# Optimization experiments

Measured on AMD Instinct MI355X. Metric: run time of the kernel, lower is better.

## Reference

```python
import jax, jax.numpy as jnp
import numpy as np

N_LIG, N_REC = 4096, 16384
E_LIG, E_REC = 65536, 262144
H, OUT, ORIG = 256, 256, 64
EF_LIG, EF_REC = 16, 16
N_SIG = 15
SLOPE = 0.01      # leakyrelu_neg_slope
SKIP_H = 0.5      # skip_weight_h
X_INIT = 0.25     # x_connection_init
SIGMAS = np.asarray(1.5 ** np.arange(N_SIG), dtype=np.float32)  # all_sigmas_dist


def _lrelu(x):
    return jax.nn.leaky_relu(x, SLOPE)


def _mlp2(x, w1, b1, w2, b2):
    # Linear -> LeakyReLU -> (Identity norm) -> Linear
    return _lrelu(x @ w1 + b1) @ w2 + b2


def _seg_mean(vals, idx, n):
    s = jax.ops.segment_sum(vals, idx, num_segments=n)
    d = jax.ops.segment_sum(jnp.ones((vals.shape[0], 1), vals.dtype), idx, num_segments=n)
    return s / jnp.maximum(d, 1.0)


def _rbf(x_rel):
    # multi-sigma RBF of squared edge distance: exp(-|x_rel|^2 / sigma), 15 sigmas
    d2 = jnp.sum(x_rel * x_rel, axis=1, keepdims=True)        # [E,1]
    return jnp.exp(-d2 / jnp.asarray(SIGMAS, x_rel.dtype))    # [E,15]


def _cross_attention(q, k, v, mask):
    a = mask * (q @ k.T) - 1000.0 * (1.0 - mask)
    return jax.nn.softmax(a, axis=1) @ v


def setup_inputs():
    key = jax.random.key(0)
    ks = iter(jax.random.split(key, 64))

    def rn(*shape):
        return jax.random.normal(next(ks), shape, dtype=jnp.float32)

    def w(fi, fo):
        return rn(fi, fo) / np.float32(np.sqrt(fi))

    e_in_l = 2 * H + EF_LIG + N_SIG
    e_in_r = 2 * H + EF_REC + N_SIG
    n_in = ORIG + H + OUT
    z = lambda d: jnp.zeros((d,), jnp.float32)
    inp = dict(
        coords_lig=rn(N_LIG, 3), h_feats_lig=rn(N_LIG, H),
        orig_lig_feats=rn(N_LIG, ORIG), orig_coords_lig=rn(N_LIG, 3),
        coords_rec=rn(N_REC, 3), h_feats_rec=rn(N_REC, H),
        orig_rec_feats=rn(N_REC, ORIG), orig_coords_rec=rn(N_REC, 3),
        mask=jnp.ones((N_LIG, N_REC), jnp.float32),
        lig_edge_feat=rn(E_LIG, EF_LIG), rec_edge_feat=rn(E_REC, EF_REC),
        lig_src=jax.random.randint(next(ks), (E_LIG,), 0, N_LIG),
        lig_dst=jax.random.randint(next(ks), (E_LIG,), 0, N_LIG),
        rec_src=jax.random.randint(next(ks), (E_REC,), 0, N_REC),
        rec_dst=jax.random.randint(next(ks), (E_REC,), 0, N_REC),
        lig_edge_w1=w(e_in_l, OUT), lig_edge_b1=z(OUT), lig_edge_w2=w(OUT, OUT), lig_edge_b2=z(OUT),
        rec_edge_w1=w(e_in_r, OUT), rec_edge_b1=z(OUT), rec_edge_w2=w(OUT, OUT), rec_edge_b2=z(OUT),
        att_q_lig_w=w(H, H), att_k_lig_w=w(H, H), att_v_lig_w=w(H, H),
        att_q_rec_w=w(H, H), att_k_rec_w=w(H, H), att_v_rec_w=w(H, H),
        node_lig_w1=w(n_in, H), node_lig_b1=z(H), node_lig_w2=w(H, OUT), node_lig_b2=z(OUT),
        node_rec_w1=w(n_in, H), node_rec_b1=z(H), node_rec_w2=w(H, OUT), node_rec_b2=z(OUT),
        coords_lig_w1=w(OUT, OUT), coords_lig_b1=z(OUT), coords_lig_w2=w(OUT, 1), coords_lig_b2=z(1),
        coords_rec_w1=w(OUT, OUT), coords_rec_b1=z(OUT), coords_rec_w2=w(OUT, 1), coords_rec_b2=z(1),
    )
    return inp


def reference(coords_lig, h_feats_lig, orig_lig_feats, orig_coords_lig,
              coords_rec, h_feats_rec, orig_rec_feats, orig_coords_rec,
              mask, lig_edge_feat, rec_edge_feat,
              lig_src, lig_dst, rec_src, rec_dst,
              lig_edge_w1, lig_edge_b1, lig_edge_w2, lig_edge_b2,
              rec_edge_w1, rec_edge_b1, rec_edge_w2, rec_edge_b2,
              att_q_lig_w, att_k_lig_w, att_v_lig_w,
              att_q_rec_w, att_k_rec_w, att_v_rec_w,
              node_lig_w1, node_lig_b1, node_lig_w2, node_lig_b2,
              node_rec_w1, node_rec_b1, node_rec_w2, node_rec_b2,
              coords_lig_w1, coords_lig_b1, coords_lig_w2, coords_lig_b2,
              coords_rec_w1, coords_rec_b1, coords_rec_w2, coords_rec_b2):
    n_lig, n_rec = coords_lig.shape[0], coords_rec.shape[0]
    # edge messages: gather endpoint features + edge attrs + RBF(dist)
    x_rel_l = coords_lig[lig_src] - coords_lig[lig_dst]                       # [E_lig,3]
    msg_l = _mlp2(jnp.concatenate([h_feats_lig[lig_src], h_feats_lig[lig_dst],
                                   lig_edge_feat, _rbf(x_rel_l)], axis=1),
                  lig_edge_w1, lig_edge_b1, lig_edge_w2, lig_edge_b2)         # [E_lig,OUT]
    x_rel_r = coords_rec[rec_src] - coords_rec[rec_dst]
    msg_r = _mlp2(jnp.concatenate([h_feats_rec[rec_src], h_feats_rec[rec_dst],
                                   rec_edge_feat, _rbf(x_rel_r)], axis=1),
                  rec_edge_w1, rec_edge_b1, rec_edge_w2, rec_edge_b2)         # [E_rec,OUT]
    # cross attention between ligand and receptor node sets
    cross_l = _cross_attention(_lrelu(h_feats_lig @ att_q_lig_w),
                               _lrelu(h_feats_rec @ att_k_rec_w),
                               h_feats_rec @ att_v_rec_w, mask)               # [N_lig,H]
    cross_r = _cross_attention(_lrelu(h_feats_rec @ att_q_rec_w),
                               _lrelu(h_feats_lig @ att_k_lig_w),
                               h_feats_lig @ att_v_lig_w, mask.T)             # [N_rec,H]
    # equivariant coordinate updates: mean over incoming edges of x_rel * coords_mlp(msg)
    x_upd_l = _seg_mean(x_rel_l * _mlp2(msg_l, coords_lig_w1, coords_lig_b1,
                                        coords_lig_w2, coords_lig_b2), lig_dst, n_lig)
    x_upd_r = _seg_mean(x_rel_r * _mlp2(msg_r, coords_rec_w1, coords_rec_b1,
                                        coords_rec_w2, coords_rec_b2), rec_dst, n_rec)
    x_ev_l = X_INIT * orig_coords_lig + (1.0 - X_INIT) * coords_lig + x_upd_l
    x_ev_r = X_INIT * orig_coords_rec + (1.0 - X_INIT) * coords_rec + x_upd_r
    # node feature updates: cat(aggr_msg, cross_att, original features) -> MLP + skip
    aggr_l = _seg_mean(msg_l, lig_dst, n_lig)
    aggr_r = _seg_mean(msg_r, rec_dst, n_rec)
    h_l = SKIP_H * _mlp2(jnp.concatenate([aggr_l, cross_l, orig_lig_feats], axis=1),
                         node_lig_w1, node_lig_b1, node_lig_w2, node_lig_b2) \
          + (1.0 - SKIP_H) * h_feats_lig
    h_r = SKIP_H * _mlp2(jnp.concatenate([aggr_r, cross_r, orig_rec_feats], axis=1),
                         node_rec_w1, node_rec_b1, node_rec_w2, node_rec_b2) \
          + (1.0 - SKIP_H) * h_feats_rec
    return (x_ev_l, h_l, x_ev_r, h_r)
```

## Files before the change

kernel.cpp:

```cpp
#include <hip/hip_runtime.h>
#include <hip/hip_bf16.h>


#define N_LIG   4096
#define N_REC   16384
#define E_LIG_N 65536
#define E_REC_N 262144
#define HD      256
#define ORIGD   64
#define EFD     16
#define NSIG    15
#define EIN     543
#define XP      552
#define XPN     584
#define XPP     264
#define FP      264

typedef __bf16 bf16x8 __attribute__((ext_vector_type(8)));
typedef float  f32x4  __attribute__((ext_vector_type(4)));

__device__ __forceinline__ float lrelu(float x) { return x > 0.f ? x : 0.01f * x; }
__device__ __forceinline__ unsigned short f2bu(float f) {
    __hip_bfloat16 h = __float2bfloat16(f);
    return *reinterpret_cast<unsigned short*>(&h);
}

__device__ __forceinline__ void glds16(const void* g, void* l) {
    __builtin_amdgcn_global_load_lds(
        (const __attribute__((address_space(1))) void*)g,
        (__attribute__((address_space(3))) void*)l,
        16, 0, 0);
}

__device__ __forceinline__ void stage_tile(
    const __hip_bfloat16* g, unsigned short* l, int wave, int lane)
{
    #pragma unroll
    for (int i = 0; i < 2; ++i) {
        const __hip_bfloat16* gp = g + (size_t)(i * 512 + wave * 64 + lane) * 8;
        unsigned short* lp = l + (i * 512 + wave * 64) * 8;
        glds16(gp, lp);
    }
}

__device__ __forceinline__ void mfma_gemm(
    const unsigned short* sA, int pitch,
    const __hip_bfloat16* Wswz, int KS, int lane, f32x4 acc[2][4])
{
    const int col = lane & 15, quad = lane >> 4;
    const unsigned short* a0p = sA + (size_t)col * pitch + quad * 8;
    const unsigned short* a1p = sA + (size_t)(16 + col) * pitch + quad * 8;
    const __hip_bfloat16* wp = Wswz + lane * 8;

    bf16x8 bE[4], bO[4], aE0, aE1, aO0, aO1;
    #pragma unroll
    for (int nt = 0; nt < 4; ++nt) {
        bE[nt] = *reinterpret_cast<const bf16x8*>(wp + (size_t)nt * KS * 512);
        bO[nt] = *reinterpret_cast<const bf16x8*>(wp + ((size_t)nt * KS + 1) * 512);
    }
    aE0 = *reinterpret_cast<const bf16x8*>(a0p);
    aE1 = *reinterpret_cast<const bf16x8*>(a1p);
    aO0 = *reinterpret_cast<const bf16x8*>(a0p + 32);
    aO1 = *reinterpret_cast<const bf16x8*>(a1p + 32);

    int ks = 0;
    for (; ks + 2 <= KS; ks += 2) {
        #pragma unroll
        for (int nt = 0; nt < 4; ++nt) {
            acc[0][nt] = __builtin_amdgcn_mfma_f32_16x16x32_bf16(aE0, bE[nt], acc[0][nt], 0, 0, 0);
            acc[1][nt] = __builtin_amdgcn_mfma_f32_16x16x32_bf16(aE1, bE[nt], acc[1][nt], 0, 0, 0);
        }
        if (ks + 2 < KS) {
            #pragma unroll
            for (int nt = 0; nt < 4; ++nt)
                bE[nt] = *reinterpret_cast<const bf16x8*>(
                    wp + ((size_t)nt * KS + ks + 2) * 512);
            aE0 = *reinterpret_cast<const bf16x8*>(a0p + (ks + 2) * 32);
            aE1 = *reinterpret_cast<const bf16x8*>(a1p + (ks + 2) * 32);
        }
        #pragma unroll
        for (int nt = 0; nt < 4; ++nt) {
            acc[0][nt] = __builtin_amdgcn_mfma_f32_16x16x32_bf16(aO0, bO[nt], acc[0][nt], 0, 0, 0);
            acc[1][nt] = __builtin_amdgcn_mfma_f32_16x16x32_bf16(aO1, bO[nt], acc[1][nt], 0, 0, 0);
        }
        if (ks + 3 < KS) {
            #pragma unroll
            for (int nt = 0; nt < 4; ++nt)
                bO[nt] = *reinterpret_cast<const bf16x8*>(
                    wp + ((size_t)nt * KS + ks + 3) * 512);
            aO0 = *reinterpret_cast<const bf16x8*>(a0p + (ks + 3) * 32);
            aO1 = *reinterpret_cast<const bf16x8*>(a1p + (ks + 3) * 32);
        }
    }
    if (ks < KS) {
        #pragma unroll
        for (int nt = 0; nt < 4; ++nt) {
            acc[0][nt] = __builtin_amdgcn_mfma_f32_16x16x32_bf16(aE0, bE[nt], acc[0][nt], 0, 0, 0);
            acc[1][nt] = __builtin_amdgcn_mfma_f32_16x16x32_bf16(aE1, bE[nt], acc[1][nt], 0, 0, 0);
        }
    }
}

__global__ void zero_kernel(float* __restrict__ p, int n) {
    int i = blockIdx.x * 256 + threadIdx.x;
    if (i < n) p[i] = 0.f;
}

__global__ void f2b_kernel(const float* __restrict__ src,
                           __hip_bfloat16* __restrict__ dst, int n8) {
    const int i = blockIdx.x * 256 + threadIdx.x;
    if (i >= n8) return;
    const float4 a = *reinterpret_cast<const float4*>(src + (size_t)i * 8);
    const float4 b = *reinterpret_cast<const float4*>(src + (size_t)i * 8 + 4);
    ushort4 u0 = { f2bu(a.x), f2bu(a.y), f2bu(a.z), f2bu(a.w) };
    ushort4 u1 = { f2bu(b.x), f2bu(b.y), f2bu(b.z), f2bu(b.w) };
    unsigned short* d = (unsigned short*)dst + (size_t)i * 8;
    *reinterpret_cast<ushort4*>(d)     = u0;
    *reinterpret_cast<ushort4*>(d + 4) = u1;
}

__global__ void hist_kernel(const int* __restrict__ dst, int* __restrict__ hist, int n) {
    int i = blockIdx.x * 256 + threadIdx.x;
    if (i < n) atomicAdd(&hist[dst[i]], 1);
}

__global__ __launch_bounds__(256) void scan_kernel(
    const int* __restrict__ hist, int* __restrict__ cur,
    float* __restrict__ cntf, int n)
{
    __shared__ int part[256];
    const int tid = threadIdx.x;
    const int per = n >> 8;
    const int base = tid * per;
    int s = 0;
    for (int i = 0; i < per; ++i) s += hist[base + i];
    part[tid] = s;
    __syncthreads();
    #pragma unroll
    for (int off = 1; off < 256; off <<= 1) {
        int v = (tid >= off) ? part[tid - off] : 0;
        __syncthreads();
        part[tid] += v;
        __syncthreads();
    }
    int run = part[tid] - s;
    for (int i = 0; i < per; ++i) {
        const int h = hist[base + i];
        cur[base + i]  = run;
        cntf[base + i] = (float)h;
        run += h;
    }
}

__global__ void scatter_kernel(const int* __restrict__ dst, int* __restrict__ cur,
                               int* __restrict__ elist, int n) {
    int i = blockIdx.x * 256 + threadIdx.x;
    if (i < n) { int p = atomicAdd(&cur[dst[i]], 1); elist[p] = i; }
}

__global__ void wt_swz(const float* __restrict__ src,
                       __hip_bfloat16* __restrict__ dst, int K, int KS) {
    const int g  = blockIdx.x / KS;
    const int ks = blockIdx.x % KS;
    for (int i = threadIdx.x; i < 512; i += 256) {
        const int lane = i >> 3, j = i & 7;
        const int n = g * 16 + (lane & 15);
        const int k = ks * 32 + (lane >> 4) * 8 + j;
        const float v = (k < K) ? src[(size_t)k * 256 + n] : 0.f;
        dst[((size_t)(g * KS + ks) * 64 + lane) * 8 + j] = __float2bfloat16(v);
    }
}

__global__ __launch_bounds__(256, 4) void edge_mfma(
    const float* __restrict__ coords, const __hip_bfloat16* __restrict__ hb,
    const __hip_bfloat16* __restrict__ efb,
    const int* __restrict__ src, const int* __restrict__ dst,
    const int* __restrict__ elist,
    const __hip_bfloat16* __restrict__ W1s, const float* __restrict__ b1,
    const __hip_bfloat16* __restrict__ W2s, const float* __restrict__ b2,
    const __hip_bfloat16* __restrict__ Wc1s, const float* __restrict__ bc1,
    const float* __restrict__ wc2v, const float* __restrict__ bc2,
    float* __restrict__ aggr, float* __restrict__ xsum)
{
    __shared__ unsigned short sX[32][XP];
    __shared__ float sXrel[32][3];
    __shared__ int   sDst[32];
    __shared__ int   sSrc[32];
    __shared__ int   sE[32];
    __shared__ float sRedW[4][32];
    __shared__ float sPv[32];

    const int tid  = threadIdx.x;
    const int lane = tid & 63;
    const int wave = tid >> 6;
    const int col  = lane & 15;
    const int quad = lane >> 4;
    const int e0   = blockIdx.x * 32;

    if (tid < 32) {
        const int e = elist[e0 + tid];
        const int s = src[e], d = dst[e];
        sE[tid] = e; sSrc[tid] = s; sDst[tid] = d;
        float d2 = 0.f;
        #pragma unroll
        for (int c = 0; c < 3; ++c) {
            const float xr = coords[s * 3 + c] - coords[d * 3 + c];
            sXrel[tid][c] = xr;
            d2 += xr * xr;
        }
        float sig = 1.0f;
        #pragma unroll
        for (int si = 0; si < NSIG; ++si) {
            sX[tid][528 + si] = f2bu(__expf(-d2 / sig));
            sig *= 1.5f;
        }
        sX[tid][543] = 0;
    }
    __syncthreads();

    for (int i = tid; i < 32 * 64; i += 256) {
        const int row = i >> 6, c = i & 63;
        const int node = (c < 32) ? sSrc[row] : sDst[row];
        const int chunk = c & 31;
        *reinterpret_cast<uint4*>(&sX[row][(c < 32 ? 0 : 256) + chunk * 8]) =
            *reinterpret_cast<const uint4*>(&hb[(size_t)node * HD + chunk * 8]);
    }
    if (tid < 64) {
        const int row = tid >> 1, hh = tid & 1;
        *reinterpret_cast<uint4*>(&sX[row][512 + hh * 8]) =
            *reinterpret_cast<const uint4*>(&efb[(size_t)sE[row] * EFD + hh * 8]);
    }
    __syncthreads();

    f32x4 acc[2][4];
    f32x4 macc[2][4];

    #pragma unroll
    for (int nt = 0; nt < 4; ++nt) {
        const float bv = b1[wave * 64 + nt * 16 + col];
        acc[0][nt] = { bv, bv, bv, bv };
        acc[1][nt] = { bv, bv, bv, bv };
    }
    mfma_gemm(&sX[0][0], XP, W1s + (size_t)(wave * 4) * 17 * 512, 17, lane, acc);
    __syncthreads();
    #pragma unroll
    for (int mt = 0; mt < 2; ++mt)
        #pragma unroll
        for (int nt = 0; nt < 4; ++nt)
            #pragma unroll
            for (int r = 0; r < 4; ++r)
                sX[mt * 16 + quad * 4 + r][wave * 64 + nt * 16 + col] =
                    f2bu(lrelu(acc[mt][nt][r]));
    __syncthreads();

    #pragma unroll
    for (int nt = 0; nt < 4; ++nt) {
        const float bv = b2[wave * 64 + nt * 16 + col];
        macc[0][nt] = { bv, bv, bv, bv };
        macc[1][nt] = { bv, bv, bv, bv };
    }
    mfma_gemm(&sX[0][0], XP, W2s + (size_t)(wave * 4) * 8 * 512, 8, lane, macc);
    __syncthreads();
    #pragma unroll
    for (int mt = 0; mt < 2; ++mt)
        #pragma unroll
        for (int nt = 0; nt < 4; ++nt)
            #pragma unroll
            for (int r = 0; r < 4; ++r)
                sX[mt * 16 + quad * 4 + r][wave * 64 + nt * 16 + col] =
                    f2bu(macc[mt][nt][r]);
    __syncthreads();

    #pragma unroll
    for (int nt = 0; nt < 4; ++nt) {
        const float bv = bc1[wave * 64 + nt * 16 + col];
        acc[0][nt] = { bv, bv, bv, bv };
        acc[1][nt] = { bv, bv, bv, bv };
    }
    mfma_gemm(&sX[0][0], XP, Wc1s + (size_t)(wave * 4) * 8 * 512, 8, lane, acc);
    float w2l[4];
    #pragma unroll
    for (int nt = 0; nt < 4; ++nt) w2l[nt] = wc2v[wave * 64 + nt * 16 + col];
    #pragma unroll
    for (int mt = 0; mt < 2; ++mt) {
        float pr[4] = { 0.f, 0.f, 0.f, 0.f };
        #pragma unroll
        for (int nt = 0; nt < 4; ++nt)
            #pragma unroll
            for (int r = 0; r < 4; ++r)
                pr[r] += lrelu(acc[mt][nt][r]) * w2l[nt];
        #pragma unroll
        for (int r = 0; r < 4; ++r) {
            #pragma unroll
            for (int off = 1; off < 16; off <<= 1) pr[r] += __shfl_xor(pr[r], off);
        }
        if (col == 0)
            #pragma unroll
            for (int r = 0; r < 4; ++r)
                sRedW[wave][mt * 16 + quad * 4 + r] = pr[r];
    }
    __syncthreads();

    float* sF = reinterpret_cast<float*>(&sX[0][0]);
    #pragma unroll
    for (int mt = 0; mt < 2; ++mt)
        #pragma unroll
        for (int nt = 0; nt < 4; ++nt)
            #pragma unroll
            for (int r = 0; r < 4; ++r)
                sF[(mt * 16 + quad * 4 + r) * FP + wave * 64 + nt * 16 + col] =
                    macc[mt][nt][r];
    if (tid < 32)
        sPv[tid] = sRedW[0][tid] + sRedW[1][tid] + sRedW[2][tid] + sRedW[3][tid]
                 + bc2[0];
    __syncthreads();

    {
        const int c = tid;
        float av = 0.f;
        int dprev = sDst[0];
        for (int row = 0; row < 32; ++row) {
            const int d = sDst[row];
            if (d != dprev) {
                atomicAdd(&aggr[(size_t)dprev * HD + c], av);
                av = 0.f; dprev = d;
            }
// ... 79 lines not shown
            for (int r = 0; r < 4; ++r)
                sXn[mt * 16 + quad * 4 + r][wave * 64 + nt * 16 + col] =
                    f2bu(lrelu(acc[mt][nt][r]));
    __syncthreads();

    #pragma unroll
    for (int nt = 0; nt < 4; ++nt) {
        const float bv = b2[wave * 64 + nt * 16 + col];
        acc[0][nt] = { bv, bv, bv, bv };
        acc[1][nt] = { bv, bv, bv, bv };
    }
    mfma_gemm(&sXn[0][0], XPN, WN2s + (size_t)(wave * 4) * 8 * 512, 8, lane, acc);
    #pragma unroll
    for (int mt = 0; mt < 2; ++mt)
        #pragma unroll
        for (int nt = 0; nt < 4; ++nt)
            #pragma unroll
            for (int r = 0; r < 4; ++r) {
                const int g = r0 + mt * 16 + quad * 4 + r;
                const int n = wave * 64 + nt * 16 + col;
                out[(size_t)g * HD + n] =
                    0.5f * acc[mt][nt][r] + 0.5f * hfeat[(size_t)g * HD + n];
            }
}

__global__ __launch_bounds__(256, 4) void qkv_proj(
    const __hip_bfloat16* __restrict__ Xb,
    const __hip_bfloat16* __restrict__ Wq, const __hip_bfloat16* __restrict__ Wk,
    const __hip_bfloat16* __restrict__ Wv,
    __hip_bfloat16* __restrict__ Q, __hip_bfloat16* __restrict__ Kz,
    __hip_bfloat16* __restrict__ Vz)
{
    __shared__ unsigned short sXp[32][XPP];
    const int tid  = threadIdx.x;
    const int lane = tid & 63;
    const int wave = tid >> 6;
    const int col  = lane & 15;
    const int quad = lane >> 4;
    const int r0   = blockIdx.x * 32;

    for (int i = tid; i < 32 * 32; i += 256) {
        const int row = i >> 5, c = i & 31;
        *reinterpret_cast<uint4*>(&sXp[row][c * 8]) =
            *reinterpret_cast<const uint4*>(&Xb[(size_t)(r0 + row) * HD + c * 8]);
    }
    __syncthreads();

    f32x4 acc[2][4];
    #pragma unroll
    for (int p = 0; p < 3; ++p) {
        const __hip_bfloat16* Ws = (p == 0) ? Wq : (p == 1) ? Wk : Wv;
        #pragma unroll
        for (int nt = 0; nt < 4; ++nt) {
            acc[0][nt] = { 0.f, 0.f, 0.f, 0.f };
            acc[1][nt] = { 0.f, 0.f, 0.f, 0.f };
        }
        mfma_gemm(&sXp[0][0], XPP, Ws + (size_t)(wave * 4) * 8 * 512, 8, lane, acc);
        #pragma unroll
        for (int mt = 0; mt < 2; ++mt)
            #pragma unroll
            for (int nt = 0; nt < 4; ++nt)
                #pragma unroll
                for (int r = 0; r < 4; ++r) {
                    float v = acc[mt][nt][r];
                    const int row = r0 + mt * 16 + quad * 4 + r;
                    const int c   = wave * 64 + nt * 16 + col;
                    if (p == 0) {
                        Q[(size_t)row * HD + c] = __float2bfloat16(lrelu(v));
                    } else if (p == 1) {
                        const int kt = row >> 4, rr = row & 15;
                        const int s  = c >> 5, cc8 = (c >> 3) & 3, j = c & 7;
                        Kz[(size_t)(kt * 8 + s) * 512 + (cc8 * 16 + rr) * 8 + j] =
                            __float2bfloat16(lrelu(v));
                    } else {
                        const int jt = row >> 5, rowin = row & 31;
                        const int dt = c >> 4, cc = c & 15;
                        Vz[((size_t)(jt * 16 + dt) * 64 + (rowin >> 3) * 16 + cc) * 8
                           + (rowin & 7)] = __float2bfloat16(v);
                    }
                }
    }
}

__device__ __forceinline__ void load_mask(
    const float* __restrict__ maskG, int transposed, int R0, int j0,
    int wave, int quad, int col, float mv[2][4])
{
    if (!transposed) {
        #pragma unroll
        for (int t = 0; t < 2; ++t)
            #pragma unroll
            for (int r = 0; r < 4; ++r)
                mv[t][r] = maskG[(size_t)(R0 + wave * 16 + quad * 4 + r) * N_REC
                                 + j0 + col + 16 * t];
    } else {
        #pragma unroll
        for (int t = 0; t < 2; ++t)
            #pragma unroll
            for (int r = 0; r < 4; ++r)
                mv[t][r] = maskG[(size_t)(j0 + col + 16 * t) * N_REC
                                 + R0 + wave * 16 + quad * 4 + r];
    }
}

__device__ __forceinline__ void attn_tile(
    const unsigned short* sK, const unsigned short* sV,
    unsigned short (*sPw)[40], const bf16x8 qf[8], const float mv[2][4],
    int lane, int col, int quad, f32x4 o[16], float m[4], float l[4])
{
    f32x4 sacc[2];
    sacc[0][0]=0.f; sacc[0][1]=0.f; sacc[0][2]=0.f; sacc[0][3]=0.f;
    sacc[1][0]=0.f; sacc[1][1]=0.f; sacc[1][2]=0.f; sacc[1][3]=0.f;
    #pragma unroll
    for (int t = 0; t < 2; ++t) {
        #pragma unroll
        for (int s = 0; s < 8; ++s) {
            bf16x8 kf = *reinterpret_cast<const bf16x8*>(
                &sK[(t * 8 + s) * 512 + lane * 8]);
            sacc[t] = __builtin_amdgcn_mfma_f32_16x16x32_bf16(qf[s], kf, sacc[t], 0, 0, 0);
        }
    }

    float a[2][4];
    #pragma unroll
    for (int t = 0; t < 2; ++t)
        #pragma unroll
        for (int r = 0; r < 4; ++r)
            a[t][r] = mv[t][r] * sacc[t][r] - 1000.f * (1.f - mv[t][r]);

    float lm[4];
    #pragma unroll
    for (int r = 0; r < 4; ++r) lm[r] = fmaxf(a[0][r], a[1][r]);
    float w = lm[0] - m[0];
    #pragma unroll
    for (int r = 1; r < 4; ++r) w = fmaxf(w, lm[r] - m[r]);
    if (!__all(w <= 8.f)) {
        #pragma unroll
        for (int r = 0; r < 4; ++r) {
            float mx = lm[r];
            #pragma unroll
            for (int off = 1; off < 16; off <<= 1)
                mx = fmaxf(mx, __shfl_xor(mx, off));
            const float mn = fmaxf(m[r], mx);
            const float c  = __expf(m[r] - mn);
            m[r] = mn;
            l[r] *= c;
            #pragma unroll
            for (int dt = 0; dt < 16; ++dt) o[dt][r] *= c;
        }
    }

    #pragma unroll
    for (int r = 0; r < 4; ++r) {
        const float p0 = __expf(a[0][r] - m[r]);
        const float p1 = __expf(a[1][r] - m[r]);
        sPw[quad * 4 + r][col]      = f2bu(p0);
        sPw[quad * 4 + r][col + 16] = f2bu(p1);
        l[r] += p0 + p1;
    }

    bf16x8 pf = *reinterpret_cast<const bf16x8*>(&sPw[col][quad * 8]);
    #pragma unroll
    for (int dt = 0; dt < 16; ++dt) {
        bf16x8 vf = *reinterpret_cast<const bf16x8*>(&sV[dt * 512 + lane * 8]);
        o[dt] = __builtin_amdgcn_mfma_f32_16x16x32_bf16(pf, vf, o[dt], 0, 0, 0);
    }
}

__global__ __launch_bounds__(512) void attn_mfma(
    const __hip_bfloat16* __restrict__ Qb, const __hip_bfloat16* __restrict__ Kz,
    const __hip_bfloat16* __restrict__ Vz, const float* __restrict__ maskG,
    float* __restrict__ PO, float* __restrict__ PM, float* __restrict__ PL,
    int M, int chunkKeys, int transposed)
{
    __shared__ unsigned short sKb[2][8192];
    __shared__ unsigned short sVb[2][8192];
    __shared__ unsigned short sP[8][16][40];

    const int tid  = threadIdx.x;
    const int lane = tid & 63;
    const int wave = tid >> 6;
    const int col  = lane & 15;
    const int quad = lane >> 4;
    const int R0   = blockIdx.x * 128;
    const int split = blockIdx.y;
    const int jbase = split * chunkKeys;

    bf16x8 qf[8];
    {
        const __hip_bfloat16* qp =
            Qb + (size_t)(R0 + wave * 16 + col) * HD + quad * 8;
        #pragma unroll
        for (int s = 0; s < 8; ++s)
            qf[s] = *reinterpret_cast<const bf16x8*>(qp + 32 * s);
    }

    f32x4 o[16];
    #pragma unroll
    for (int dt = 0; dt < 16; ++dt) { o[dt][0]=0.f; o[dt][1]=0.f; o[dt][2]=0.f; o[dt][3]=0.f; }
    float m[4], l[4];
    #pragma unroll
    for (int r = 0; r < 4; ++r) { m[r] = -INFINITY; l[r] = 0.f; }

    float mvA[2][4], mvB[2][4];

    stage_tile(Kz + (size_t)jbase * 256, &sKb[0][0], wave, lane);
    stage_tile(Vz + (size_t)jbase * 256, &sVb[0][0], wave, lane);
    load_mask(maskG, transposed, R0, jbase, wave, quad, col, mvA);

    for (int jt = 0; jt < chunkKeys; jt += 64) {
        asm volatile("s_waitcnt vmcnt(0)" ::: "memory");
        __builtin_amdgcn_s_barrier();
        __builtin_amdgcn_sched_barrier(0);
        stage_tile(Kz + (size_t)(jbase + jt + 32) * 256, &sKb[1][0], wave, lane);
        stage_tile(Vz + (size_t)(jbase + jt + 32) * 256, &sVb[1][0], wave, lane);
        load_mask(maskG, transposed, R0, jbase + jt + 32, wave, quad, col, mvB);
        __builtin_amdgcn_sched_barrier(0);
        attn_tile(&sKb[0][0], &sVb[0][0], sP[wave], qf, mvA,
                  lane, col, quad, o, m, l);

        asm volatile("s_waitcnt vmcnt(0)" ::: "memory");
        __builtin_amdgcn_s_barrier();
        __builtin_amdgcn_sched_barrier(0);
        if (jt + 64 < chunkKeys) {
            stage_tile(Kz + (size_t)(jbase + jt + 64) * 256, &sKb[0][0], wave, lane);
            stage_tile(Vz + (size_t)(jbase + jt + 64) * 256, &sVb[0][0], wave, lane);
            load_mask(maskG, transposed, R0, jbase + jt + 64, wave, quad, col, mvA);
        }
        __builtin_amdgcn_sched_barrier(0);
        attn_tile(&sKb[1][0], &sVb[1][0], sP[wave], qf, mvB,
                  lane, col, quad, o, m, l);
    }

    #pragma unroll
    for (int r = 0; r < 4; ++r) {
        #pragma unroll
        for (int off = 1; off < 16; off <<= 1)
            l[r] += __shfl_xor(l[r], off);
    }

    #pragma unroll
    for (int dt = 0; dt < 16; ++dt)
        #pragma unroll
        for (int r = 0; r < 4; ++r) {
            const int row = R0 + wave * 16 + quad * 4 + r;
            PO[((size_t)split * M + row) * HD + dt * 16 + col] = o[dt][r];
        }
    if (col == 0) {
        #pragma unroll
        for (int r = 0; r < 4; ++r) {
            const int row = R0 + wave * 16 + quad * 4 + r;
            PM[(size_t)split * M + row] = m[r];
            PL[(size_t)split * M + row] = l[r];
        }
    }
}

__global__ void attn_combine(
    const float* __restrict__ PO, const float* __restrict__ PM,
    const float* __restrict__ PL, __hip_bfloat16* __restrict__ Out,
    int M, int nchunks)
{
    const int idx = blockIdx.x * 256 + threadIdx.x;
    const int row = idx >> 8;
    float mmax = -INFINITY;
    for (int c = 0; c < nchunks; ++c) mmax = fmaxf(mmax, PM[(size_t)c * M + row]);
    float denom = 0.f, acc = 0.f;
    for (int c = 0; c < nchunks; ++c) {
        const float w = __expf(PM[(size_t)c * M + row] - mmax);
        denom += PL[(size_t)c * M + row] * w;
        acc   += PO[(size_t)c * M * HD + idx] * w;
    }
    Out[idx] = __float2bfloat16(acc / denom);
}

__global__ void coords_fin(
    const float* __restrict__ coords, const float* __restrict__ origc,
    const float* __restrict__ xsum, const float* __restrict__ cnt,
    float* __restrict__ out, int n)
{
    const int i = blockIdx.x * 256 + threadIdx.x;
    if (i >= n * 3) return;
    const int node = i / 3;
    const float inv = 1.f / fmaxf(cnt[node], 1.f);
    out[i] = 0.25f * origc[i] + 0.75f * coords[i] + xsum[i] * inv;
}

extern "C" void kernel_launch(void* const* d_in, const int* in_sizes, int n_in,
                              void* d_out, int out_size, void* d_ws, size_t ws_size,
                              hipStream_t stream)
{
    const float* coords_lig = (const float*)d_in[0];
    const float* h_lig      = (const float*)d_in[1];
    const float* orig_lig   = (const float*)d_in[2];
    const float* origc_lig  = (const float*)d_in[3];
    const float* coords_rec = (const float*)d_in[4];
    const float* h_rec      = (const float*)d_in[5];
    const float* orig_rec   = (const float*)d_in[6];
    const float* origc_rec  = (const float*)d_in[7];
    const float* mask       = (const float*)d_in[8];
    const float* lig_ef     = (const float*)d_in[9];
    const float* rec_ef     = (const float*)d_in[10];
    const int* lig_src = (const int*)d_in[11];
    const int* lig_dst = (const int*)d_in[12];
    const int* rec_src = (const int*)d_in[13];
    const int* rec_dst = (const int*)d_in[14];
    const float* le_w1 = (const float*)d_in[15];
    const float* le_b1 = (const float*)d_in[16];
    const float* le_w2 = (const float*)d_in[17];
    const float* le_b2 = (const float*)d_in[18];
    const float* re_w1 = (const float*)d_in[19];
    const float* re_b1 = (const float*)d_in[20];
    const float* re_w2 = (const float*)d_in[21];
    const float* re_b2 = (const float*)d_in[22];
    const float* aql_w = (const float*)d_in[23];
    const float* akl_w = (const float*)d_in[24];
    const float* avl_w = (const float*)d_in[25];
    const float* aqr_w = (const float*)d_in[26];
    const float* akr_w = (const float*)d_in[27];
    const float* avr_w = (const float*)d_in[28];
    const float* nl_w1 = (const float*)d_in[29];
    const float* nl_b1 = (const float*)d_in[30];
    const float* nl_w2 = (const float*)d_in[31];
    const float* nl_b2 = (const float*)d_in[32];
    const float* nr_w1 = (const float*)d_in[33];
    const float* nr_b1 = (const float*)d_in[34];
    const float* nr_w2 = (const float*)d_in[35];
    const float* nr_b2 = (const float*)d_in[36];
    const float* cl_w1 = (const float*)d_in[37];
    const float* cl_b1 = (const float*)d_in[38];
    const float* cl_w2 = (const float*)d_in[39];
    const float* cl_b2 = (const float*)d_in[40];
    const float* cr_w1 = (const float*)d_in[41];
    const float* cr_b1 = (const float*)d_in[42];
    const float* cr_w2 = (const float*)d_in[43];
    const float* cr_b2 = (const float*)d_in[44];

    float* out = (float*)d_out;
    float* wsf = (float*)d_ws;

    const size_t AGGRL = 0;
    const size_t AGGRR = AGGRL + (size_t)N_LIG * HD;
    const size_t CNTL  = AGGRR + (size_t)N_REC * HD;
    const size_t CNTR  = CNTL + N_LIG;
    const size_t XSUML = CNTR + N_REC;
    const size_t XSUMR = XSUML + (size_t)N_LIG * 3;
    const size_t HISTL = XSUMR + (size_t)N_REC * 3;
    const size_t CURL  = HISTL + N_LIG;
    const size_t HISTR = CURL + N_LIG;
    const size_t CURR  = HISTR + N_REC;
    const size_t ZEND  = CURR + N_REC;
    const size_t ELISTL = ZEND;
    const size_t ELISTR = ELISTL + E_LIG_N;
    const size_t FEND   = ELISTR + E_REC_N;

    __hip_bfloat16* wsb = (__hip_bfloat16*)(wsf + FEND);
    const size_t QL  = 0;
    const size_t KL  = QL + (size_t)N_LIG * HD;
    const size_t VL  = KL + (size_t)N_LIG * HD;
    const size_t QR  = VL + (size_t)N_LIG * HD;
    const size_t KR  = QR + (size_t)N_REC * HD;
    const size_t VR  = KR + (size_t)N_REC * HD;
    const size_t CRL = VR + (size_t)N_REC * HD;
    const size_t CRR = CRL + (size_t)N_LIG * HD;
    const size_t KZL = CRR + (size_t)N_REC * HD;
    const size_t VZL = KZL + (size_t)N_LIG * HD;
    const size_t KZR = VZL + (size_t)N_LIG * HD;
    const size_t VZR = KZR + (size_t)N_REC * HD;
    const size_t EW1SZ = (size_t)16 * 17 * 512;
    const size_t KW256 = (size_t)16 * 8 * 512;
    const size_t NW1SZ = (size_t)16 * 18 * 512;
    const size_t SW_EL1 = VZR + (size_t)N_REC * HD;
    const size_t SW_EL2 = SW_EL1 + EW1SZ;
    const size_t SW_EC1 = SW_EL2 + KW256;
    const size_t SW_NL1 = SW_EC1 + KW256;
    const size_t SW_NL2 = SW_NL1 + NW1SZ;
    const size_t SW_ER1 = SW_NL2 + KW256;
    const size_t SW_ER2 = SW_ER1 + EW1SZ;
    const size_t SW_EC1R = SW_ER2 + KW256;
    const size_t SW_NR1 = SW_EC1R + KW256;
    const size_t SW_NR2 = SW_NR1 + NW1SZ;
    const size_t SW_PQL = SW_NR2 + KW256;
    const size_t SW_PKL = SW_PQL + KW256;
    const size_t SW_PVL = SW_PKL + KW256;
    const size_t SW_PQR = SW_PVL + KW256;
    const size_t SW_PKR = SW_PQR + KW256;
    const size_t SW_PVR = SW_PKR + KW256;
    const size_t HB_L  = SW_PVR + KW256;
    const size_t HB_R  = HB_L + (size_t)N_LIG * HD;
    const size_t EFB_L = HB_R + (size_t)N_REC * HD;
    const size_t EFB_R = EFB_L + (size_t)E_LIG_N * EFD;
    const size_t BF_END = EFB_R + (size_t)E_REC_N * EFD;

    float* wsp = (float*)(wsb + ((BF_END + 1) & ~(size_t)1));
    const size_t baseBytes = (size_t)((char*)wsp - (char*)d_ws);
    int SL = 16, SR = 4;
    {
        const size_t poElems16 = (size_t)16 * N_LIG * HD;
        const size_t need16 = baseBytes +
            (poElems16 + 2 * (size_t)16 * N_LIG) * sizeof(float);
        if (ws_size < need16) { SL = 8; SR = 2; }
    }
    const size_t PO_ = 0;
    const size_t PM_ = PO_ + (size_t)SL * N_LIG * HD;
    const size_t PL_ = PM_ + (size_t)SL * N_LIG;

    const size_t O_XL = 0;
    const size_t O_HL = O_XL + (size_t)N_LIG * 3;
    const size_t O_XR = O_HL + (size_t)N_LIG * HD;
    const size_t O_HR = O_XR + (size_t)N_REC * 3;

    zero_kernel<<<((int)ZEND + 255) / 256, 256, 0, stream>>>(wsf, (int)ZEND);

    f2b_kernel<<<(N_LIG * HD / 8 + 255) / 256, 256, 0, stream>>>(
        h_lig, wsb + HB_L, N_LIG * HD / 8);
    f2b_kernel<<<(N_REC * HD / 8 + 255) / 256, 256, 0, stream>>>(
        h_rec, wsb + HB_R, N_REC * HD / 8);
    f2b_kernel<<<(E_LIG_N * EFD / 8 + 255) / 256, 256, 0, stream>>>(
        lig_ef, wsb + EFB_L, E_LIG_N * EFD / 8);
    f2b_kernel<<<(E_REC_N * EFD / 8 + 255) / 256, 256, 0, stream>>>(
        rec_ef, wsb + EFB_R, E_REC_N * EFD / 8);

    hist_kernel<<<E_LIG_N / 256, 256, 0, stream>>>(lig_dst, (int*)(wsf + HISTL), E_LIG_N);
    hist_kernel<<<E_REC_N / 256, 256, 0, stream>>>(rec_dst, (int*)(wsf + HISTR), E_REC_N);
    scan_kernel<<<1, 256, 0, stream>>>((int*)(wsf + HISTL), (int*)(wsf + CURL),
                                       wsf + CNTL, N_LIG);
    scan_kernel<<<1, 256, 0, stream>>>((int*)(wsf + HISTR), (int*)(wsf + CURR),
                                       wsf + CNTR, N_REC);
    scatter_kernel<<<E_LIG_N / 256, 256, 0, stream>>>(
        lig_dst, (int*)(wsf + CURL), (int*)(wsf + ELISTL), E_LIG_N);
    scatter_kernel<<<E_REC_N / 256, 256, 0, stream>>>(
        rec_dst, (int*)(wsf + CURR), (int*)(wsf + ELISTR), E_REC_N);

    wt_swz<<<16 * 17, 256, 0, stream>>>(le_w1, wsb + SW_EL1, EIN, 17);
    wt_swz<<<16 * 8,  256, 0, stream>>>(le_w2, wsb + SW_EL2, 256, 8);
    wt_swz<<<16 * 8,  256, 0, stream>>>(cl_w1, wsb + SW_EC1, 256, 8);
    wt_swz<<<16 * 18, 256, 0, stream>>>(nl_w1, wsb + SW_NL1, 576, 18);
    wt_swz<<<16 * 8,  256, 0, stream>>>(nl_w2, wsb + SW_NL2, 256, 8);
    wt_swz<<<16 * 17, 256, 0, stream>>>(re_w1, wsb + SW_ER1, EIN, 17);
    wt_swz<<<16 * 8,  256, 0, stream>>>(re_w2, wsb + SW_ER2, 256, 8);
    wt_swz<<<16 * 8,  256, 0, stream>>>(cr_w1, wsb + SW_EC1R, 256, 8);
    wt_swz<<<16 * 18, 256, 0, stream>>>(nr_w1, wsb + SW_NR1, 576, 18);
    wt_swz<<<16 * 8,  256, 0, stream>>>(nr_w2, wsb + SW_NR2, 256, 8);
    wt_swz<<<16 * 8,  256, 0, stream>>>(aql_w, wsb + SW_PQL, 256, 8);
    wt_swz<<<16 * 8,  256, 0, stream>>>(akl_w, wsb + SW_PKL, 256, 8);
    wt_swz<<<16 * 8,  256, 0, stream>>>(avl_w, wsb + SW_PVL, 256, 8);
    wt_swz<<<16 * 8,  256, 0, stream>>>(aqr_w, wsb + SW_PQR, 256, 8);
    wt_swz<<<16 * 8,  256, 0, stream>>>(akr_w, wsb + SW_PKR, 256, 8);
    wt_swz<<<16 * 8,  256, 0, stream>>>(avr_w, wsb + SW_PVR, 256, 8);

    edge_mfma<<<E_LIG_N / 32, 256, 0, stream>>>(
        coords_lig, wsb + HB_L, wsb + EFB_L, lig_src, lig_dst,
        (const int*)(wsf + ELISTL),
        wsb + SW_EL1, le_b1, wsb + SW_EL2, le_b2, wsb + SW_EC1, cl_b1, cl_w2, cl_b2,
        wsf + AGGRL, wsf + XSUML);
    edge_mfma<<<E_REC_N / 32, 256, 0, stream>>>(
        coords_rec, wsb + HB_R, wsb + EFB_R, rec_src, rec_dst,
        (const int*)(wsf + ELISTR),
        wsb + SW_ER1, re_b1, wsb + SW_ER2, re_b2, wsb + SW_EC1R, cr_b1, cr_w2, cr_b2,
        wsf + AGGRR, wsf + XSUMR);

    qkv_proj<<<N_LIG / 32, 256, 0, stream>>>(
        wsb + HB_L, wsb + SW_PQL, wsb + SW_PKL, wsb + SW_PVL,
        wsb + QL, wsb + KZL, wsb + VZL);
    qkv_proj<<<N_REC / 32, 256, 0, stream>>>(
        wsb + HB_R, wsb + SW_PQR, wsb + SW_PKR, wsb + SW_PVR,
        wsb + QR, wsb + KZR, wsb + VZR);

    {
        dim3 gl(N_LIG / 128, SL);
        attn_mfma<<<gl, 512, 0, stream>>>(wsb + QL, wsb + KZR, wsb + VZR, mask,
                                          wsp + PO_, wsp + PM_, wsp + PL_,
                                          N_LIG, N_REC / SL, 0);
        attn_combine<<<N_LIG, 256, 0, stream>>>(
            wsp + PO_, wsp + PM_, wsp + PL_, wsb + CRL, N_LIG, SL);

        dim3 gr(N_REC / 128, SR);
        attn_mfma<<<gr, 512, 0, stream>>>(wsb + QR, wsb + KZL, wsb + VZL, mask,
                                          wsp + PO_, wsp + PM_, wsp + PL_,
                                          N_REC, N_LIG / SR, 1);
        attn_combine<<<N_REC, 256, 0, stream>>>(
            wsp + PO_, wsp + PM_, wsp + PL_, wsb + CRR, N_REC, SR);
    }

    coords_fin<<<(N_LIG * 3 + 255) / 256, 256, 0, stream>>>(
        coords_lig, origc_lig, wsf + XSUML, wsf + CNTL, out + O_XL, N_LIG);
    coords_fin<<<(N_REC * 3 + 255) / 256, 256, 0, stream>>>(
        coords_rec, origc_rec, wsf + XSUMR, wsf + CNTR, out + O_XR, N_REC);

    node_mfma<<<N_LIG / 32, 256, 0, stream>>>(
        wsf + AGGRL, wsf + CNTL, wsb + CRL, orig_lig, h_lig,
        wsb + SW_NL1, nl_b1, wsb + SW_NL2, nl_b2, out + O_HL);
    node_mfma<<<N_REC / 32, 256, 0, stream>>>(
        wsf + AGGRR, wsf + CNTR, wsb + CRR, orig_rec, h_rec,
        wsb + SW_NR1, nr_b1, wsb + SW_NR2, nr_b2, out + O_HR);

    (void)in_sizes; (void)n_in; (void)out_size;
}
```

Baseline: 1.299 ms.

## Precompute per-node src/dst projections of edge MLP first layer

Splits the edge MLP's first-layer weight into src-node, dst-node and tail (edge features plus RBF) parts. A new hproj kernel computes the h_src·W and h_dst·W products once per node, and the edge kernel gathers and adds these fp32 rows. Only the small 32-wide tail is still multiplied per edge with one MFMA step. This removes most of the per-edge first-layer GEMM, since there are far more edges than nodes. In exchange, the edge kernel gathers twice as many bytes per edge (fp32 instead of bf16), and it needs extra workspace plus an extra launch.

Result: slower. 1.343 ms (+3.4%).

```diff
diff --git a/kernel.cpp b/kernel.cpp
--- a/kernel.cpp
+++ b/kernel.cpp
@@ -15,6 +15,7 @@
 #define XPN     584
 #define XPP     264
 #define FP      264
+#define FPH     276
 
 typedef __bf16 bf16x8 __attribute__((ext_vector_type(8)));
 typedef float  f32x4  __attribute__((ext_vector_type(4)));
@@ -171,18 +172,62 @@
     }
 }
 
+__global__ __launch_bounds__(256, 4) void hproj(
+    const __hip_bfloat16* __restrict__ Xb,
+    const __hip_bfloat16* __restrict__ Wsrc, const __hip_bfloat16* __restrict__ Wdst,
+    float* __restrict__ HS, float* __restrict__ HDp)
+{
+    __shared__ unsigned short sXp[32][XPP];
+    const int tid  = threadIdx.x;
+    const int lane = tid & 63;
+    const int wave = tid >> 6;
+    const int col  = lane & 15;
+    const int quad = lane >> 4;
+    const int r0   = blockIdx.x * 32;
+
+    for (int i = tid; i < 32 * 32; i += 256) {
+        const int row = i >> 5, c = i & 31;
+        *reinterpret_cast<uint4*>(&sXp[row][c * 8]) =
+            *reinterpret_cast<const uint4*>(&Xb[(size_t)(r0 + row) * HD + c * 8]);
+    }
+    __syncthreads();
+
+    f32x4 acc[2][4];
+    #pragma unroll
+    for (int p = 0; p < 2; ++p) {
+        const __hip_bfloat16* Ws = (p == 0) ? Wsrc : Wdst;
+        float* outp = (p == 0) ? HS : HDp;
+        #pragma unroll
+        for (int nt = 0; nt < 4; ++nt) {
+            acc[0][nt] = { 0.f, 0.f, 0.f, 0.f };
+            acc[1][nt] = { 0.f, 0.f, 0.f, 0.f };
+        }
+        mfma_gemm(&sXp[0][0], XPP, Ws + (size_t)(wave * 4) * 8 * 512, 8, lane, acc);
+        #pragma unroll
+        for (int mt = 0; mt < 2; ++mt)
+            #pragma unroll
+            for (int nt = 0; nt < 4; ++nt)
+                #pragma unroll
+                for (int r = 0; r < 4; ++r)
+                    outp[(size_t)(r0 + mt * 16 + quad * 4 + r) * HD +
+                         wave * 64 + nt * 16 + col] = acc[mt][nt][r];
+    }
+}
+
 __global__ __launch_bounds__(256, 4) void edge_mfma(
-    const float* __restrict__ coords, const __hip_bfloat16* __restrict__ hb,
+    const float* __restrict__ coords,
+    const float* __restrict__ hs, const float* __restrict__ hd,
     const __hip_bfloat16* __restrict__ efb,
     const int* __restrict__ src, const int* __restrict__ dst,
     const int* __restrict__ elist,
-    const __hip_bfloat16* __restrict__ W1s, const float* __restrict__ b1,
+    const __hip_bfloat16* __restrict__ W1t, const float* __restrict__ b1,
     const __hip_bfloat16* __restrict__ W2s, const float* __restrict__ b2,
     const __hip_bfloat16* __restrict__ Wc1s, const float* __restrict__ bc1,
     const float* __restrict__ wc2v, const float* __restrict__ bc2,
     float* __restrict__ aggr, float* __restrict__ xsum)
 {
     __shared__ unsigned short sX[32][XP];
+    __shared__ unsigned short sT[32][40];
     __shared__ float sXrel[32][3];
     __shared__ int   sDst[32];
     __shared__ int   sSrc[32];
@@ -211,23 +256,28 @@
         float sig = 1.0f;
         #pragma unroll
         for (int si = 0; si < NSIG; ++si) {
-            sX[tid][528 + si] = f2bu(__expf(-d2 / sig));
+            sT[tid][16 + si] = f2bu(__expf(-d2 / sig));
             sig *= 1.5f;
         }
-        sX[tid][543] = 0;
-    }
-    __syncthreads();
-
+        sT[tid][31] = 0;
+    }
+    __syncthreads();
+
+    float* sXf = reinterpret_cast<float*>(&sX[0][0]);
     for (int i = tid; i < 32 * 64; i += 256) {
-        const int row = i >> 6, c = i & 63;
-        const int node = (c < 32) ? sSrc[row] : sDst[row];
-        const int chunk = c & 31;
-        *reinterpret_cast<uint4*>(&sX[row][(c < 32 ? 0 : 256) + chunk * 8]) =
-            *reinterpret_cast<const uint4*>(&hb[(size_t)node * HD + chunk * 8]);
+        const int row = i >> 6, c4 = i & 63;
+        const float4 a = *reinterpret_cast<const float4*>(
+            &hs[(size_t)sSrc[row] * HD + c4 * 4]);
+        const float4 b = *reinterpret_cast<const float4*>(
+            &hd[(size_t)sDst[row] * HD + c4 * 4]);
+        float4 sum;
+        sum.x = a.x + b.x; sum.y = a.y + b.y;
+        sum.z = a.z + b.z; sum.w = a.w + b.w;
+        *reinterpret_cast<float4*>(&sXf[row * FPH + c4 * 4]) = sum;
     }
     if (tid < 64) {
         const int row = tid >> 1, hh = tid & 1;
-        *reinterpret_cast<uint4*>(&sX[row][512 + hh * 8]) =
+        *reinterpret_cast<uint4*>(&sT[row][hh * 8]) =
             *reinterpret_cast<const uint4*>(&efb[(size_t)sE[row] * EFD + hh * 8]);
     }
     __syncthreads();
@@ -241,7 +291,25 @@
         acc[0][nt] = { bv, bv, bv, bv };
         acc[1][nt] = { bv, bv, bv, bv };
     }
-    mfma_gemm(&sX[0][0], XP, W1s + (size_t)(wave * 4) * 17 * 512, 17, lane, acc);
+    #pragma unroll
+    for (int mt = 0; mt < 2; ++mt)
+        #pragma unroll
+        for (int nt = 0; nt < 4; ++nt)
+            #pragma unroll
+            for (int r = 0; r < 4; ++r)
+                acc[mt][nt][r] +=
+                    sXf[(mt * 16 + quad * 4 + r) * FPH + wave * 64 + nt * 16 + col];
+    {
+        const bf16x8 aT0 = *reinterpret_cast<const bf16x8*>(&sT[col][quad * 8]);
+        const bf16x8 aT1 = *reinterpret_cast<const bf16x8*>(&sT[16 + col][quad * 8]);
+        #pragma unroll
+        for (int nt = 0; nt < 4; ++nt) {
+            const bf16x8 bT = *reinterpret_cast<const bf16x8*>(
+                W1t + (size_t)(wave * 4 + nt) * 512 + lane * 8);
+            acc[0][nt] = __builtin_amdgcn_mfma_f32_16x16x32_bf16(aT0, bT, acc[0][nt], 0, 0, 0);
+            acc[1][nt] = __builtin_amdgcn_mfma_f32_16x16x32_bf16(aT1, bT, acc[1][nt], 0, 0, 0);
+        }
+    }
     __syncthreads();
     #pragma unroll
     for (int mt = 0; mt < 2; ++mt)
@@ -757,7 +825,11 @@
     const size_t ZEND  = CURR + N_REC;
     const size_t ELISTL = ZEND;
     const size_t ELISTR = ELISTL + E_LIG_N;
-    const size_t FEND   = ELISTR + E_REC_N;
+    const size_t HS_L   = ELISTR + E_REC_N;
+    const size_t HD_L   = HS_L + (size_t)N_LIG * HD;
+    const size_t HS_R   = HD_L + (size_t)N_LIG * HD;
+    const size_t HD_R   = HS_R + (size_t)N_REC * HD;
+    const size_t FEND   = HD_R + (size_t)N_REC * HD;
 
     __hip_bfloat16* wsb = (__hip_bfloat16*)(wsf + FEND);
     const size_t QL  = 0;
@@ -772,16 +844,20 @@
     const size_t VZL = KZL + (size_t)N_LIG * HD;
     const size_t KZR = VZL + (size_t)N_LIG * HD;
     const size_t VZR = KZR + (size_t)N_REC * HD;
-    const size_t EW1SZ = (size_t)16 * 17 * 512;
     const size_t KW256 = (size_t)16 * 8 * 512;
+    const size_t KTAIL = (size_t)16 * 512;
     const size_t NW1SZ = (size_t)16 * 18 * 512;
-    const size_t SW_EL1 = VZR + (size_t)N_REC * HD;
-    const size_t SW_EL2 = SW_EL1 + EW1SZ;
+    const size_t SW_ESL = VZR + (size_t)N_REC * HD;
+    const size_t SW_EDL = SW_ESL + KW256;
+    const size_t SW_ETL = SW_EDL + KW256;
+    const size_t SW_EL2 = SW_ETL + KTAIL;
     const size_t SW_EC1 = SW_EL2 + KW256;
     const size_t SW_NL1 = SW_EC1 + KW256;
     const size_t SW_NL2 = SW_NL1 + NW1SZ;
-    const size_t SW_ER1 = SW_NL2 + KW256;
-    const size_t SW_ER2 = SW_ER1 + EW1SZ;
+    const size_t SW_ESR = SW_NL2 + KW256;
+    const size_t SW_EDR = SW_ESR + KW256;
+    const size_t SW_ETR = SW_EDR + KW256;
+    const size_t SW_ER2 = SW_ETR + KTAIL;
     const size_t SW_EC1R = SW_ER2 + KW256;
     const size_t SW_NR1 = SW_EC1R + KW256;
     const size_t SW_NR2 = SW_NR1 + NW1SZ;
@@ -837,12 +913,16 @@
     scatter_kernel<<<E_REC_N / 256, 256, 0, stream>>>(
         rec_dst, (int*)(wsf + CURR), (int*)(wsf + ELISTR), E_REC_N);
 
-    wt_swz<<<16 * 17, 256, 0, stream>>>(le_w1, wsb + SW_EL1, EIN, 17);
+    wt_swz<<<16 * 8,  256, 0, stream>>>(le_w1,             wsb + SW_ESL, 256, 8);
+    wt_swz<<<16 * 8,  256, 0, stream>>>(le_w1 + 256 * 256, wsb + SW_EDL, 256, 8);
+    wt_swz<<<16 * 1,  256, 0, stream>>>(le_w1 + 512 * 256, wsb + SW_ETL, 31, 1);
     wt_swz<<<16 * 8,  256, 0, stream>>>(le_w2, wsb + SW_EL2, 256, 8);
     wt_swz<<<16 * 8,  256, 0, stream>>>(cl_w1, wsb + SW_EC1, 256, 8);
     wt_swz<<<16 * 18, 256, 0, stream>>>(nl_w1, wsb + SW_NL1, 576, 18);
     wt_swz<<<16 * 8,  256, 0, stream>>>(nl_w2, wsb + SW_NL2, 256, 8);
-    wt_swz<<<16 * 17, 256, 0, stream>>>(re_w1, wsb + SW_ER1, EIN, 17);
+    wt_swz<<<16 * 8,  256, 0, stream>>>(re_w1,             wsb + SW_ESR, 256, 8);
+    wt_swz<<<16 * 8,  256, 0, stream>>>(re_w1 + 256 * 256, wsb + SW_EDR, 256, 8);
+    wt_swz<<<16 * 1,  256, 0, stream>>>(re_w1 + 512 * 256, wsb + SW_ETR, 31, 1);
     wt_swz<<<16 * 8,  256, 0, stream>>>(re_w2, wsb + SW_ER2, 256, 8);
     wt_swz<<<16 * 8,  256, 0, stream>>>(cr_w1, wsb + SW_EC1R, 256, 8);
     wt_swz<<<16 * 18, 256, 0, stream>>>(nr_w1, wsb + SW_NR1, 576, 18);
@@ -854,15 +934,20 @@
     wt_swz<<<16 * 8,  256, 0, stream>>>(akr_w, wsb + SW_PKR, 256, 8);
     wt_swz<<<16 * 8,  256, 0, stream>>>(avr_w, wsb + SW_PVR, 256, 8);
 
+    hproj<<<N_LIG / 32, 256, 0, stream>>>(
+        wsb + HB_L, wsb + SW_ESL, wsb + SW_EDL, wsf + HS_L, wsf + HD_L);
+    hproj<<<N_REC / 32, 256, 0, stream>>>(
+        wsb + HB_R, wsb + SW_ESR, wsb + SW_EDR, wsf + HS_R, wsf + HD_R);
+
     edge_mfma<<<E_LIG_N / 32, 256, 0, stream>>>(
-        coords_lig, wsb + HB_L, wsb + EFB_L, lig_src, lig_dst,
+        coords_lig, wsf + HS_L, wsf + HD_L, wsb + EFB_L, lig_src, lig_dst,
         (const int*)(wsf + ELISTL),
-        wsb + SW_EL1, le_b1, wsb + SW_EL2, le_b2, wsb + SW_EC1, cl_b1, cl_w2, cl_b2,
+        wsb + SW_ETL, le_b1, wsb + SW_EL2, le_b2, wsb + SW_EC1, cl_b1, cl_w2, cl_b2,
         wsf + AGGRL, wsf + XSUML);
     edge_mfma<<<E_REC_N / 32, 256, 0, stream>>>(
-        coords_rec, wsb + HB_R, wsb + EFB_R, rec_src, rec_dst,
+        coords_rec, wsf + HS_R, wsf + HD_R, wsb + EFB_R, rec_src, rec_dst,
         (const int*)(wsf + ELISTR),
-        wsb + SW_ER1, re_b1, wsb + SW_ER2, re_b2, wsb + SW_EC1R, cr_b1, cr_w2, cr_b2,
+        wsb + SW_ETR, re_b1, wsb + SW_ER2, re_b2, wsb + SW_EC1R, cr_b1, cr_w2, cr_b2,
         wsf + AGGRR, wsf + XSUMR);
 
     qkv_proj<<<N_LIG / 32, 256, 0, stream>>>(
```

## Precompute per-tile mask flags to skip mask loads in attention

Applied to the files above, without the earlier changes.

Adds a pre-pass that scans the dense fp32 mask once and records, per 32x32 tile, whether any entry differs from one. The attention kernels check these flags and load and apply the mask only for tiles that contain a masked entry; otherwise they use the raw scores. This removes two full passes over the 256 MB mask (one strided, in the transposed direction) in exchange for one coalesced scan plus a flag lookup per tile. The result stays correct for any mask, but the benefit depends on the mask being mostly ones, as it is in the test inputs.

Result: no change. 1.291 ms (-0.6%).

```diff
diff --git a/kernel.cpp b/kernel.cpp
--- a/kernel.cpp
+++ b/kernel.cpp
@@ -15,6 +15,7 @@
 #define XPN     584
 #define XPP     264
 #define FP      264
+#define FCOLS   (N_REC / 32)
 
 typedef __bf16 bf16x8 __attribute__((ext_vector_type(8)));
 typedef float  f32x4  __attribute__((ext_vector_type(4)));
@@ -104,6 +105,23 @@
 __global__ void zero_kernel(float* __restrict__ p, int n) {
     int i = blockIdx.x * 256 + threadIdx.x;
     if (i < n) p[i] = 0.f;
+}
+
+__global__ void scanmask_kernel(const float* __restrict__ mask,
+                                int* __restrict__ F)
+{
+    const size_t t = (size_t)blockIdx.x * 256 + threadIdx.x;
+    const int r  = (int)(t >> 10);
+    const int c0 = ((int)t & 1023) * 16;
+    const float4* p = reinterpret_cast<const float4*>(
+        &mask[(size_t)r * N_REC + c0]);
+    bool ok = true;
+    #pragma unroll
+    for (int i = 0; i < 4; ++i) {
+        const float4 v = p[i];
+        ok = ok && (v.x == 1.f) && (v.y == 1.f) && (v.z == 1.f) && (v.w == 1.f);
+    }
+    if (!ok) atomicOr(&F[(r >> 5) * FCOLS + (c0 >> 5)], 1);
 }
 
 __global__ void f2b_kernel(const float* __restrict__ src,
@@ -487,31 +505,12 @@
     }
 }
 
-__device__ __forceinline__ void load_mask(
-    const float* __restrict__ maskG, int transposed, int R0, int j0,
-    int wave, int quad, int col, float mv[2][4])
-{
-    if (!transposed) {
-        #pragma unroll
-        for (int t = 0; t < 2; ++t)
-            #pragma unroll
-            for (int r = 0; r < 4; ++r)
-                mv[t][r] = maskG[(size_t)(R0 + wave * 16 + quad * 4 + r) * N_REC
-                                 + j0 + col + 16 * t];
-    } else {
-        #pragma unroll
-        for (int t = 0; t < 2; ++t)
-            #pragma unroll
-            for (int r = 0; r < 4; ++r)
-                mv[t][r] = maskG[(size_t)(j0 + col + 16 * t) * N_REC
-                                 + R0 + wave * 16 + quad * 4 + r];
-    }
-}
-
 __device__ __forceinline__ void attn_tile(
     const unsigned short* sK, const unsigned short* sV,
-    unsigned short (*sPw)[40], const bf16x8 qf[8], const float mv[2][4],
-    int lane, int col, int quad, f32x4 o[16], float m[4], float l[4])
+    unsigned short (*sPw)[40], const bf16x8 qf[8],
+    const float* __restrict__ maskG, const int* __restrict__ Fz,
+    int transposed, int R0, int j0,
+    int lane, int wave, int col, int quad, f32x4 o[16], float m[4], float l[4])
 {
     f32x4 sacc[2];
     sacc[0][0]=0.f; sacc[0][1]=0.f; sacc[0][2]=0.f; sacc[0][3]=0.f;
@@ -526,12 +525,37 @@
         }
     }
 
+    int anyz;
+    if (!transposed) {
+        const int base = (R0 >> 5) * FCOLS + (j0 >> 5);
+        anyz = Fz[base] | Fz[base + FCOLS] | Fz[base + 2 * FCOLS]
+             | Fz[base + 3 * FCOLS];
+    } else {
+        const int base = (j0 >> 5) * FCOLS + (R0 >> 5);
+        anyz = Fz[base] | Fz[base + 1] | Fz[base + 2] | Fz[base + 3];
+    }
     float a[2][4];
-    #pragma unroll
-    for (int t = 0; t < 2; ++t)
-        #pragma unroll
-        for (int r = 0; r < 4; ++r)
-            a[t][r] = mv[t][r] * sacc[t][r] - 1000.f * (1.f - mv[t][r]);
+    if (anyz) {
+        #pragma unroll
+        for (int t = 0; t < 2; ++t)
+            #pragma unroll
+            for (int r = 0; r < 4; ++r) {
+                float mv;
+                if (!transposed)
+                    mv = maskG[(size_t)(R0 + wave * 16 + quad * 4 + r) * N_REC
+                               + j0 + col + 16 * t];
+                else
+                    mv = maskG[(size_t)(j0 + col + 16 * t) * N_REC
+                               + R0 + wave * 16 + quad * 4 + r];
+                a[t][r] = mv * sacc[t][r] - 1000.f * (1.f - mv);
+            }
+    } else {
+        #pragma unroll
+        for (int t = 0; t < 2; ++t)
+            #pragma unroll
+            for (int r = 0; r < 4; ++r)
+                a[t][r] = sacc[t][r];
+    }
 
     float lm[4];
     #pragma unroll
@@ -575,6 +599,7 @@
 __global__ __launch_bounds__(512) void attn_mfma(
     const __hip_bfloat16* __restrict__ Qb, const __hip_bfloat16* __restrict__ Kz,
     const __hip_bfloat16* __restrict__ Vz, const float* __restrict__ maskG,
+    const int* __restrict__ Fz,
     float* __restrict__ PO, float* __restrict__ PM, float* __restrict__ PL,
     int M, int chunkKeys, int transposed)
 {
@@ -607,11 +632,8 @@
     #pragma unroll
     for (int r = 0; r < 4; ++r) { m[r] = -INFINITY; l[r] = 0.f; }
 
-    float mvA[2][4], mvB[2][4];
-
     stage_tile(Kz + (size_t)jbase * 256, &sKb[0][0], wave, lane);
     stage_tile(Vz + (size_t)jbase * 256, &sVb[0][0], wave, lane);
-    load_mask(maskG, transposed, R0, jbase, wave, quad, col, mvA);
 
     for (int jt = 0; jt < chunkKeys; jt += 64) {
         asm volatile("s_waitcnt vmcnt(0)" ::: "memory");
@@ -619,10 +641,10 @@
         __builtin_amdgcn_sched_barrier(0);
         stage_tile(Kz + (size_t)(jbase + jt + 32) * 256, &sKb[1][0], wave, lane);
         stage_tile(Vz + (size_t)(jbase + jt + 32) * 256, &sVb[1][0], wave, lane);
-        load_mask(maskG, transposed, R0, jbase + jt + 32, wave, quad, col, mvB);
         __builtin_amdgcn_sched_barrier(0);
-        attn_tile(&sKb[0][0], &sVb[0][0], sP[wave], qf, mvA,
-                  lane, col, quad, o, m, l);
+        attn_tile(&sKb[0][0], &sVb[0][0], sP[wave], qf,
+                  maskG, Fz, transposed, R0, jbase + jt,
+                  lane, wave, col, quad, o, m, l);
 
         asm volatile("s_waitcnt vmcnt(0)" ::: "memory");
         __builtin_amdgcn_s_barrier();
@@ -630,11 +652,11 @@
         if (jt + 64 < chunkKeys) {
             stage_tile(Kz + (size_t)(jbase + jt + 64) * 256, &sKb[0][0], wave, lane);
             stage_tile(Vz + (size_t)(jbase + jt + 64) * 256, &sVb[0][0], wave, lane);
-            load_mask(maskG, transposed, R0, jbase + jt + 64, wave, quad, col, mvA);
         }
         __builtin_amdgcn_sched_barrier(0);
-        attn_tile(&sKb[1][0], &sVb[1][0], sP[wave], qf, mvB,
-                  lane, col, quad, o, m, l);
+        attn_tile(&sKb[1][0], &sVb[1][0], sP[wave], qf,
+                  maskG, Fz, transposed, R0, jbase + jt + 32,
+                  lane, wave, col, quad, o, m, l);
     }
 
     #pragma unroll
@@ -754,7 +776,8 @@
     const size_t CURL  = HISTL + N_LIG;
     const size_t HISTR = CURL + N_LIG;
     const size_t CURR  = HISTR + N_REC;
-    const size_t ZEND  = CURR + N_REC;
+    const size_t FLAGS = CURR + N_REC;
+    const size_t ZEND  = FLAGS + (size_t)(N_LIG / 32) * FCOLS;
     const size_t ELISTL = ZEND;
     const size_t ELISTR = ELISTL + E_LIG_N;
     const size_t FEND   = ELISTR + E_REC_N;
@@ -817,6 +840,9 @@
 
     zero_kernel<<<((int)ZEND + 255) / 256, 256, 0, stream>>>(wsf, (int)ZEND);
 
+    scanmask_kernel<<<(N_LIG * (N_REC / 16)) / 256, 256, 0, stream>>>(
+        mask, (int*)(wsf + FLAGS));
+
     f2b_kernel<<<(N_LIG * HD / 8 + 255) / 256, 256, 0, stream>>>(
         h_lig, wsb + HB_L, N_LIG * HD / 8);
     f2b_kernel<<<(N_REC * HD / 8 + 255) / 256, 256, 0, stream>>>(
@@ -875,6 +901,7 @@
     {
         dim3 gl(N_LIG / 128, SL);
         attn_mfma<<<gl, 512, 0, stream>>>(wsb + QL, wsb + KZR, wsb + VZR, mask,
+                                          (const int*)(wsf + FLAGS),
                                           wsp + PO_, wsp + PM_, wsp + PL_,
                                           N_LIG, N_REC / SL, 0);
         attn_combine<<<N_LIG, 256, 0, stream>>>(
@@ -882,6 +909,7 @@
 
         dim3 gr(N_REC / 128, SR);
         attn_mfma<<<gr, 512, 0, stream>>>(wsb + QR, wsb + KZL, wsb + VZL, mask,
+                                          (const int*)(wsf + FLAGS),
                                           wsp + PO_, wsp + PM_, wsp + PL_,
                                           N_REC, N_LIG / SR, 1);
         attn_combine<<<N_REC, 256, 0, stream>>>(
```
